# Kernel tuning notes

Measured on AMD Instinct MI355X. Metric: run time of the kernel, lower is better.

The kernel has to match this reference:

```python
import jax, jax.numpy as jnp
import numpy as np

LAMBDA_ORD = 1.0
B, C = 65536, 256


def setup_inputs() -> dict:
    key = jax.random.key(0)
    k1, k2 = jax.random.split(key)
    predictions = jax.random.normal(k1, (B, C), dtype=jnp.float32)
    targets = jax.random.randint(k2, (B,), 0, C, dtype=jnp.int64)
    return {"predictions": predictions, "targets": targets}


def reference(predictions, targets):
    # Cross-entropy with mean reduction
    logp = jax.nn.log_softmax(predictions, axis=-1)          # [B, C]
    ce = -jnp.mean(jnp.take_along_axis(logp, targets[:, None], axis=1))
    # Ordinal penalty: mean_i sum_j softmax(pred_i)_j * (j - t_i)^2
    probs = jnp.exp(logp)                                     # [B, C]
    j = jnp.arange(predictions.shape[1], dtype=predictions.dtype)  # [C]
    dist2 = (j[None, :] - targets[:, None].astype(predictions.dtype)) ** 2  # [B, C]
    penalty = jnp.mean(jnp.sum(probs * dist2, axis=-1))
    return ce + LAMBDA_ORD * penalty
```

## Files before the change

### kernel.cpp

```cpp
#include <hip/hip_runtime.h>

#define NROWS  65536
#define NCLS   256
#define NBLK   2048

__global__ __launch_bounds__(256) void OrdinalLoss_main_kernel(
    const float* __restrict__ pred, const int* __restrict__ tgt,
    float* __restrict__ partial, int nrows)
{
    const int tid    = blockIdx.x * blockDim.x + threadIdx.x;
    const int lane   = threadIdx.x & 63;
    const int g      = lane >> 4;
    const int li     = lane & 15;
    const int wave   = tid >> 6;
    const int nwaves = (gridDim.x * blockDim.x) >> 6;

    float acc = 0.0f;

    if (tid < nrows)
        acc = -pred[(size_t)tid * NCLS + tgt[tid]];

    const int npacks = nrows >> 2;
    for (int pack = wave; pack < npacks; pack += nwaves) {
        const int row = pack * 4 + g;
        const float* rp = pred + (size_t)row * NCLS + li * 4;

        const float4 p0 = *reinterpret_cast<const float4*>(rp);
        const float4 p1 = *reinterpret_cast<const float4*>(rp + 64);
        const float4 p2 = *reinterpret_cast<const float4*>(rp + 128);
        const float4 p3 = *reinterpret_cast<const float4*>(rp + 192);
        const float tf  = (float)tgt[row];
        const float j0  = (float)(li * 4);

        float s = 0.0f, w = 0.0f;
        #define TERM(pv, col) { float e = __expf(pv); s += e;              \
                                float d = (col) - tf; w = fmaf(e * d, d, w); }
        TERM(p0.x, j0 +   0.0f) TERM(p0.y, j0 +   1.0f)
        TERM(p0.z, j0 +   2.0f) TERM(p0.w, j0 +   3.0f)
        TERM(p1.x, j0 +  64.0f) TERM(p1.y, j0 +  65.0f)
        TERM(p1.z, j0 +  66.0f) TERM(p1.w, j0 +  67.0f)
        TERM(p2.x, j0 + 128.0f) TERM(p2.y, j0 + 129.0f)
        TERM(p2.z, j0 + 130.0f) TERM(p2.w, j0 + 131.0f)
        TERM(p3.x, j0 + 192.0f) TERM(p3.y, j0 + 193.0f)
        TERM(p3.z, j0 + 194.0f) TERM(p3.w, j0 + 195.0f)
        #undef TERM

        #pragma unroll
        for (int m = 8; m; m >>= 1) {
            s += __shfl_xor(s, m);
            w += __shfl_xor(w, m);
        }
        if (li == 0)
            acc += __logf(s) + w / s;
    }

    __shared__ float red[256];
    red[threadIdx.x] = acc;
    __syncthreads();
    if (threadIdx.x < 64) {
        float v = red[threadIdx.x] + red[threadIdx.x + 64] +
                  red[threadIdx.x + 128] + red[threadIdx.x + 192];
        #pragma unroll
        for (int mask = 32; mask; mask >>= 1)
            v += __shfl_xor(v, mask);
        if (threadIdx.x == 0)
            partial[blockIdx.x] = v;
    }
}

__global__ __launch_bounds__(256) void OrdinalLoss_final_kernel(
    const float* __restrict__ partial, float* __restrict__ out)
{
    float v = 0.0f;
    #pragma unroll
    for (int i = 0; i < NBLK / 256; ++i)
        v += partial[threadIdx.x + i * 256];

    __shared__ float red[256];
    red[threadIdx.x] = v;
    __syncthreads();
    if (threadIdx.x < 64) {
        float s = red[threadIdx.x] + red[threadIdx.x + 64] +
                  red[threadIdx.x + 128] + red[threadIdx.x + 192];
        #pragma unroll
        for (int mask = 32; mask; mask >>= 1)
            s += __shfl_xor(s, mask);
        if (threadIdx.x == 0)
            out[0] = s * (1.0f / (float)NROWS);
    }
}

extern "C" void kernel_launch(void* const* d_in, const int* in_sizes, int n_in,
                              void* d_out, int out_size, void* d_ws, size_t ws_size,
                              hipStream_t stream) {
    const float* pred = (const float*)d_in[0];
    const int*   tgt  = (const int*)d_in[1];
    float*       out  = (float*)d_out;
    float*       ws   = (float*)d_ws;
    const int nrows   = in_sizes[1];

    OrdinalLoss_main_kernel<<<NBLK, 256, 0, stream>>>(pred, tgt, ws, nrows);
    OrdinalLoss_final_kernel<<<1, 256, 0, stream>>>(ws, out);
}
```

Before: 19.53 us.

## Unroll two row-packs per wave and expand squared distance into moment sums

The main loop now handles two row-packs per iteration, issuing eight float4 loads before any math so more memory requests are in flight per wave. The ordinal term (j-t)^2 is expanded into three per-row moment sums (sum e, sum e*j, sum e*j^2), using precomputed column constants so the per-element work no longer depends on the target. The target-logit gather moves to lanes 0-7 of each wave in a grid-strided loop. The cost is more registers, and the expanded form can lose some float precision through cancellation.

```diff
diff --git a/kernel.cpp b/kernel.cpp
--- a/kernel.cpp
+++ b/kernel.cpp
@@ -17,42 +17,85 @@
 
     float acc = 0.0f;
 
-    if (tid < nrows)
-        acc = -pred[(size_t)tid * NCLS + tgt[tid]];
+    if (lane < 8) {
+        for (int r = wave * 8 + lane; r < nrows; r += nwaves * 8)
+            acc = -pred[(size_t)r * NCLS + tgt[r]];
+    }
+
+    const float j0 = (float)(li * 4);
+    float c[16], c2[16];
+    #pragma unroll
+    for (int k = 0; k < 16; ++k) {
+        const float col = j0 + (float)((k >> 2) * 64 + (k & 3));
+        c[k]  = col;
+        c2[k] = col * col;
+    }
+
+    #define TERM(S0, S1, S2, PV, K) { float e = __expf(PV); S0 += e;        \
+                                      S1 = fmaf(e, c[K],  S1);              \
+                                      S2 = fmaf(e, c2[K], S2); }
+    #define PACK16(S0, S1, S2, Q0, Q1, Q2, Q3)                              \
+        TERM(S0,S1,S2, Q0.x, 0)  TERM(S0,S1,S2, Q0.y, 1)                    \
+        TERM(S0,S1,S2, Q0.z, 2)  TERM(S0,S1,S2, Q0.w, 3)                    \
+        TERM(S0,S1,S2, Q1.x, 4)  TERM(S0,S1,S2, Q1.y, 5)                    \
+        TERM(S0,S1,S2, Q1.z, 6)  TERM(S0,S1,S2, Q1.w, 7)                    \
+        TERM(S0,S1,S2, Q2.x, 8)  TERM(S0,S1,S2, Q2.y, 9)                    \
+        TERM(S0,S1,S2, Q2.z,10)  TERM(S0,S1,S2, Q2.w,11)                    \
+        TERM(S0,S1,S2, Q3.x,12)  TERM(S0,S1,S2, Q3.y,13)                    \
+        TERM(S0,S1,S2, Q3.z,14)  TERM(S0,S1,S2, Q3.w,15)
+
+    #define REDUCE_ROW(S0, S1, S2, T)                                       \
+        _Pragma("unroll")                                                   \
+        for (int m = 8; m; m >>= 1) {                                       \
+            S0 += __shfl_xor(S0, m);                                        \
+            S1 += __shfl_xor(S1, m);                                        \
+            S2 += __shfl_xor(S2, m);                                        \
+        }                                                                   \
+        if (li == 0) {                                                      \
+            const float tf = (float)(T);                                    \
+            acc += __logf(S0) + (S2 - 2.0f * tf * S1 + tf * tf * S0) / S0;  \
+        }
 
     const int npacks = nrows >> 2;
-    for (int pack = wave; pack < npacks; pack += nwaves) {
-        const int row = pack * 4 + g;
-        const float* rp = pred + (size_t)row * NCLS + li * 4;
+    int pack = wave;
+    for (; pack + nwaves < npacks; pack += 2 * nwaves) {
+        const int rowA = pack * 4 + g;
+        const int rowB = (pack + nwaves) * 4 + g;
+        const float* rpA = pred + (size_t)rowA * NCLS + li * 4;
+        const float* rpB = pred + (size_t)rowB * NCLS + li * 4;
+        const float4 a0 = *reinterpret_cast<const float4*>(rpA);
+        const float4 a1 = *reinterpret_cast<const float4*>(rpA + 64);
+        const float4 a2 = *reinterpret_cast<const float4*>(rpA + 128);
+        const float4 a3 = *reinterpret_cast<const float4*>(rpA + 192);
+        const float4 b0 = *reinterpret_cast<const float4*>(rpB);
+        const float4 b1 = *reinterpret_cast<const float4*>(rpB + 64);
+        const float4 b2 = *reinterpret_cast<const float4*>(rpB + 128);
+        const float4 b3 = *reinterpret_cast<const float4*>(rpB + 192);
+        const int tA = tgt[rowA];
+        const int tB = tgt[rowB];
 
-        const float4 p0 = *reinterpret_cast<const float4*>(rp);
-        const float4 p1 = *reinterpret_cast<const float4*>(rp + 64);
-        const float4 p2 = *reinterpret_cast<const float4*>(rp + 128);
-        const float4 p3 = *reinterpret_cast<const float4*>(rp + 192);
-        const float tf  = (float)tgt[row];
-        const float j0  = (float)(li * 4);
-
-        float s = 0.0f, w = 0.0f;
-        #define TERM(pv, col) { float e = __expf(pv); s += e;              \
-                                float d = (col) - tf; w = fmaf(e * d, d, w); }
-        TERM(p0.x, j0 +   0.0f) TERM(p0.y, j0 +   1.0f)
-        TERM(p0.z, j0 +   2.0f) TERM(p0.w, j0 +   3.0f)
-        TERM(p1.x, j0 +  64.0f) TERM(p1.y, j0 +  65.0f)
-        TERM(p1.z, j0 +  66.0f) TERM(p1.w, j0 +  67.0f)
-        TERM(p2.x, j0 + 128.0f) TERM(p2.y, j0 + 129.0f)
-        TERM(p2.z, j0 + 130.0f) TERM(p2.w, j0 + 131.0f)
-        TERM(p3.x, j0 + 192.0f) TERM(p3.y, j0 + 193.0f)
-        TERM(p3.z, j0 + 194.0f) TERM(p3.w, j0 + 195.0f)
-        #undef TERM
-
-        #pragma unroll
-        for (int m = 8; m; m >>= 1) {
-            s += __shfl_xor(s, m);
-            w += __shfl_xor(w, m);
-        }
-        if (li == 0)
-            acc += __logf(s) + w / s;
+        float sA0 = 0.0f, sA1 = 0.0f, sA2 = 0.0f;
+        float sB0 = 0.0f, sB1 = 0.0f, sB2 = 0.0f;
+        PACK16(sA0, sA1, sA2, a0, a1, a2, a3)
+        PACK16(sB0, sB1, sB2, b0, b1, b2, b3)
+        REDUCE_ROW(sA0, sA1, sA2, tA)
+        REDUCE_ROW(sB0, sB1, sB2, tB)
     }
+    if (pack < npacks) {
+        const int rowA = pack * 4 + g;
+        const float* rpA = pred + (size_t)rowA * NCLS + li * 4;
+        const float4 a0 = *reinterpret_cast<const float4*>(rpA);
+        const float4 a1 = *reinterpret_cast<const float4*>(rpA + 64);
+        const float4 a2 = *reinterpret_cast<const float4*>(rpA + 128);
+        const float4 a3 = *reinterpret_cast<const float4*>(rpA + 192);
+        const int tA = tgt[rowA];
+        float sA0 = 0.0f, sA1 = 0.0f, sA2 = 0.0f;
+        PACK16(sA0, sA1, sA2, a0, a1, a2, a3)
+        REDUCE_ROW(sA0, sA1, sA2, tA)
+    }
+    #undef TERM
+    #undef PACK16
+    #undef REDUCE_ROW
 
     __shared__ float red[256];
     red[threadIdx.x] = acc;
```

Measured after the change: 19.88 us. About the same (+1.8%).
